# Optimization experiments

Measured on AMD Instinct MI355X. Metric: run time of the kernel, lower is better.

The kernel has to match this reference:

```python
import jax, jax.numpy as jnp
import numpy as np
import math

D_MODEL, N_HEAD, N_KV_HEAD, MAX_LEN = 2048, 32, 8, 2048
D_K = D_MODEL // N_HEAD
BASE = 10000.0
B, T = 2, 2048


def _rope_tables(seq_len):
    # matches torch Rotary: cos/sin of shape [seq_len, D_K], repeat_interleave(2) over freq dim
    inv_freq = 1.0 / (BASE ** (jnp.arange(0, D_K, 2, dtype=jnp.float32) / D_K))
    t = jnp.arange(seq_len, dtype=jnp.float32)[:, None] * inv_freq  # [T, D_K/2]
    cos = jnp.repeat(jnp.cos(t), 2, axis=-1)  # [T, D_K]
    sin = jnp.repeat(jnp.sin(t), 2, axis=-1)
    return cos, sin


def _rotate_half(x):
    # faithful to source: x1 = even lanes, x2 = odd lanes, concat([-x2, x1], -1)
    x1, x2 = x[..., ::2], x[..., 1::2]
    return jnp.concatenate([-x2, x1], axis=-1)


def _apply_rope(x, cos, sin):
    return x * cos + _rotate_half(x) * sin


def setup_inputs() -> dict:
    key = jax.random.key(0)
    ks = jax.random.split(key, 5)
    s = 1.0 / math.sqrt(D_MODEL)
    x = jax.random.normal(ks[0], (B, T, D_MODEL), dtype=jnp.float32)
    Wq = jax.random.normal(ks[1], (D_MODEL, N_HEAD * D_K), dtype=jnp.float32) * s
    Wk = jax.random.normal(ks[2], (D_MODEL, N_KV_HEAD * D_K), dtype=jnp.float32) * s
    Wv = jax.random.normal(ks[3], (D_MODEL, N_KV_HEAD * D_K), dtype=jnp.float32) * s
    Wo = jax.random.normal(ks[4], (N_HEAD * D_K, D_MODEL), dtype=jnp.float32) * s
    mask = jnp.tril(jnp.ones((T, T), dtype=bool))  # causal
    return {"x": x, "mask": mask, "Wq": Wq, "Wk": Wk, "Wv": Wv, "Wo": Wo}


def reference(x, mask, Wq, Wk, Wv, Wo):
    b, t, _ = x.shape
    g = N_HEAD // N_KV_HEAD
    q = (x @ Wq).reshape(b, t, N_HEAD, D_K).transpose(0, 2, 1, 3)      # [B,H,T,d]
    k = (x @ Wk).reshape(b, t, N_KV_HEAD, D_K).transpose(0, 2, 1, 3)   # [B,Hkv,T,d]
    v = (x @ Wv).reshape(b, t, N_KV_HEAD, D_K).transpose(0, 2, 1, 3)
    cos, sin = _rope_tables(t)
    q = _apply_rope(q, cos, sin)
    k = _apply_rope(k, cos, sin)  # rope before/after repeat is identical per-head
    # grouped attention: q head h attends kv head h // g (repeat_interleave semantics)
    qg = q.reshape(b, N_KV_HEAD, g, t, D_K)
    scores = jnp.einsum("bkgtd,bksd->bkgts", qg, k) / math.sqrt(D_K)
    neg = jnp.finfo(scores.dtype).min
    scores = jnp.where(mask[None, None, None, :, :], scores, neg)
    attn = jax.nn.softmax(scores, axis=-1)
    out = jnp.einsum("bkgts,bksd->bkgtd", attn, v)
    out = out.reshape(b, N_HEAD, t, D_K).transpose(0, 2, 1, 3).reshape(b, t, N_HEAD * D_K)
    return out @ Wo
```

## Files before the change

kernel.cpp:

```cpp
#include <hip/hip_runtime.h>
#include <cstdint>
#include <cstddef>

typedef unsigned short u16;
typedef __attribute__((ext_vector_type(8))) short bf16x8;
typedef __attribute__((ext_vector_type(8))) unsigned short u16x8;
typedef __attribute__((ext_vector_type(4))) unsigned short u16x4;
typedef __attribute__((ext_vector_type(4))) float f32x4;

__device__ __forceinline__ unsigned short f2bf(float f) {
    union { float f; uint32_t u; } c; c.f = f;
    uint32_t u = c.u + 0x7fffu + ((c.u >> 16) & 1u);
    return (unsigned short)(u >> 16);
}
__device__ __forceinline__ float bf2f(unsigned short h) {
    union { uint32_t u; float f; } c; c.u = ((uint32_t)h) << 16;
    return c.f;
}
__device__ __forceinline__ uint32_t pkbf(float a, float b) {
    union { float f; uint32_t u; } x, y; x.f = a; y.f = b;
    return ((x.u + 0x8000u) >> 16) | ((y.u + 0x8000u) & 0xFFFF0000u);
}

#define GLDS16(g, l)                                                               \
    __builtin_amdgcn_global_load_lds((const __attribute__((address_space(1))) void*)(g), \
                                     (__attribute__((address_space(3))) void*)(l), 16, 0, 0)

__global__ __launch_bounds__(256) void cvt_x(const float* __restrict__ src,
                                             u16* __restrict__ dst) {
    int i = blockIdx.x * 256 + threadIdx.x;
    const float4* s = (const float4*)src + (size_t)i * 2;
    float4 a = s[0], b = s[1];
    u16x8 o;
    o[0] = f2bf(a.x); o[1] = f2bf(a.y); o[2] = f2bf(a.z); o[3] = f2bf(a.w);
    o[4] = f2bf(b.x); o[5] = f2bf(b.y); o[6] = f2bf(b.z); o[7] = f2bf(b.w);
    *(u16x8*)(dst + (size_t)i * 8) = o;
}

__global__ __launch_bounds__(256) void tcvt(const float* __restrict__ src,
                                            u16* __restrict__ dst, int C) {
    __shared__ u16 tile[32][33];
    const int t = threadIdx.x;
    const int bx = blockIdx.x, by = blockIdx.y;
    const int tr = t >> 3, tc = (t & 7) << 2;
    float4 f = *(const float4*)&src[(size_t)(by * 32 + tr) * C + bx * 32 + tc];
    tile[tr][tc + 0] = f2bf(f.x); tile[tr][tc + 1] = f2bf(f.y);
    tile[tr][tc + 2] = f2bf(f.z); tile[tr][tc + 3] = f2bf(f.w);
    __syncthreads();
    u16x4 o;
    o[0] = tile[tc + 0][tr]; o[1] = tile[tc + 1][tr];
    o[2] = tile[tc + 2][tr]; o[3] = tile[tc + 3][tr];
    *(u16x4*)&dst[(size_t)(bx * 32 + tr) * 2048 + by * 32 + tc] = o;
}

__global__ __launch_bounds__(256) void tcvt3(const float* __restrict__ Wq,
                                             const float* __restrict__ Wk,
                                             const float* __restrict__ Wv,
                                             u16* __restrict__ dst) {
    __shared__ u16 tile[32][33];
    const int t = threadIdx.x;
    const int bxg = blockIdx.x, by = blockIdx.y;
    const float* src; int C, nb; u16* dbase;
    if (bxg < 64)      { src = Wq; C = 2048; nb = bxg;      dbase = dst; }
    else if (bxg < 80) { src = Wk; C = 512;  nb = bxg - 64; dbase = dst + (size_t)2048 * 2048; }
    else               { src = Wv; C = 512;  nb = bxg - 80; dbase = dst + (size_t)2560 * 2048; }
    const int tr = t >> 3, tc = (t & 7) << 2;
    float4 f = *(const float4*)&src[(size_t)(by * 32 + tr) * C + nb * 32 + tc];
    tile[tr][tc + 0] = f2bf(f.x); tile[tr][tc + 1] = f2bf(f.y);
    tile[tr][tc + 2] = f2bf(f.z); tile[tr][tc + 3] = f2bf(f.w);
    __syncthreads();
    u16x4 o;
    o[0] = tile[tc + 0][tr]; o[1] = tile[tc + 1][tr];
    o[2] = tile[tc + 2][tr]; o[3] = tile[tc + 3][tr];
    *(u16x4*)&dbase[(size_t)(nb * 32 + tr) * 2048 + by * 32 + tc] = o;
}

template <int MODE>
__global__ __launch_bounds__(256) void gemm2(const u16* __restrict__ A,
                                             const u16* __restrict__ Bt,
                                             u16* __restrict__ oq, u16* __restrict__ ok,
                                             u16* __restrict__ ov, float* __restrict__ of) {
    __shared__ u16 As[128 * 32];
    __shared__ u16 Bs[128 * 32];
    const int t = threadIdx.x, w = t >> 6, lane = t & 63;
    const int l15 = lane & 15, quad = lane >> 4;
    const int m0 = blockIdx.y << 7, n0 = blockIdx.x << 7;
    const int K = 2048;
    const int c0 = w * 2, c1 = c0 + 1;
    const int ar0 = c0 * 16 + (lane >> 2), ar1 = c1 * 16 + (lane >> 2);
    const int ac = (lane & 3) << 3;
    const u16* Ap0 = A + (size_t)(m0 + ar0) * K + ac;
    const u16* Ap1 = A + (size_t)(m0 + ar1) * K + ac;
    const u16* Bp0 = Bt + (size_t)(n0 + ar0) * K + ac;
    const u16* Bp1 = Bt + (size_t)(n0 + ar1) * K + ac;
    const int wm = (w >> 1) << 6, wn = (w & 1) << 6;

    f32x4 acc[4][4] = {};

    for (int k0 = 0; k0 < K; k0 += 32) {
        GLDS16(Ap0 + k0, &As[c0 * 512]);
        GLDS16(Ap1 + k0, &As[c1 * 512]);
        GLDS16(Bp0 + k0, &Bs[c0 * 512]);
        GLDS16(Bp1 + k0, &Bs[c1 * 512]);
        __syncthreads();
        bf16x8 a[4], bfr[4];
#pragma unroll
        for (int mt = 0; mt < 4; ++mt)
            a[mt] = *(bf16x8*)&As[(wm + mt * 16 + l15) * 32 + quad * 8];
#pragma unroll
        for (int nt = 0; nt < 4; ++nt)
            bfr[nt] = *(bf16x8*)&Bs[(wn + nt * 16 + l15) * 32 + quad * 8];
#pragma unroll
        for (int mt = 0; mt < 4; ++mt)
#pragma unroll
            for (int nt = 0; nt < 4; ++nt)
                acc[mt][nt] = __builtin_amdgcn_mfma_f32_16x16x32_bf16(a[mt], bfr[nt], acc[mt][nt], 0, 0, 0);
        __syncthreads();
    }

    if constexpr (MODE == 0) {
        const int colbase = n0 + wn;
        const bool isv = (colbase >= 2560);
        float iv[4];
        if (!isv) {
#pragma unroll
            for (int nt = 0; nt < 4; ++nt)
                iv[nt] = exp2f(-0.4152410118609253f * (float)(nt * 8 + (l15 >> 1)));
        }
        const int map1 = (quad << 4) | ((2 * l15 + 1) & 15);
        const int map2 = (quad << 4) | ((2 * l15) & 15);
        const bool lo = (l15 < 8);
#pragma unroll
        for (int mt = 0; mt < 4; ++mt)
#pragma unroll
            for (int r = 0; r < 4; ++r) {
                const int row = m0 + wm + mt * 16 + quad * 4 + r;
                float v0 = acc[mt][0][r], v1 = acc[mt][1][r];
                float v2 = acc[mt][2][r], v3 = acc[mt][3][r];
                float o0 = v0, o1 = v1, o2 = v2, o3 = v3;
                if (!isv) {
                    float g1a = __shfl(v0, map1), g1b = __shfl(v1, map1);
                    float g1c = __shfl(v2, map1), g1d = __shfl(v3, map1);
                    float g2a = __shfl(v0, map2), g2b = __shfl(v1, map2);
                    float g2c = __shfl(v2, map2), g2d = __shfl(v3, map2);
                    float p0 = lo ? g1a : g1b;
                    float p1 = lo ? g1c : g1d;
                    float p2 = lo ? g2a : g2b;
                    float p3 = lo ? g2c : g2d;
                    const float tt = (float)(row & 2047);
                    float sn, cs;
                    __sincosf(tt * iv[0], &sn, &cs); o0 = v0 * cs - p0 * sn;
                    __sincosf(tt * iv[1], &sn, &cs); o1 = v1 * cs - p1 * sn;
                    __sincosf(tt * iv[2], &sn, &cs); o2 = v2 * cs + p2 * sn;
                    __sincosf(tt * iv[3], &sn, &cs); o3 = v3 * cs + p3 * sn;
                }
                float o[4] = {o0, o1, o2, o3};
                if (colbase < 2048) {
#pragma unroll
                    for (int nt = 0; nt < 4; ++nt)
                        oq[(size_t)row * 2048 + colbase + nt * 16 + l15] = f2bf(o[nt]);
                } else if (colbase < 2560) {
#pragma unroll
                    for (int nt = 0; nt < 4; ++nt)
                        ok[(size_t)row * 512 + colbase - 2048 + nt * 16 + l15] = f2bf(o[nt]);
                } else {
#pragma unroll
                    for (int nt = 0; nt < 4; ++nt)
                        ov[(size_t)(colbase - 2560 + nt * 16 + l15) * 4096 + row] = f2bf(o[nt]);
                }
            }
    } else {
#pragma unroll
        for (int mt = 0; mt < 4; ++mt)
#pragma unroll
            for (int nt = 0; nt < 4; ++nt)
#pragma unroll
                for (int r = 0; r < 4; ++r) {
                    int row = m0 + wm + mt * 16 + quad * 4 + r;
                    int col = n0 + wn + nt * 16 + l15;
                    of[(size_t)row * 2048 + col] = acc[mt][nt][r];
                }
    }
}

__global__ __launch_bounds__(256, 3) void attn4(const u16* __restrict__ q,
                                                const u16* __restrict__ k,
                                                const u16* __restrict__ vT,
                                                u16* __restrict__ att) {
    __shared__ u16 Ks[64 * 72];
    __shared__ u16 Vt[64 * 72];
    __shared__ u16 Pw[4][16 * 72];

    const int t = threadIdx.x, w = t >> 6, lane = t & 63;
    const int l15 = lane & 15, quad = lane >> 4;
    const int bx = blockIdx.x, kvh = blockIdx.y, b = blockIdx.z;
    const int h = kvh * 4 + w;
    const size_t rowbase = (size_t)b * 2048;
    const int sr = t >> 2, sd = (t & 3) << 4;
    u16* Pq = &Pw[w][0];
    const float SC = 0.125f * 1.4426950408889634f;

    const u16* kbase = &k[(rowbase + sr) * 512 + kvh * 64 + sd];
    const u16* vbase = &vT[(size_t)(kvh * 64 + sr) * 4096 + rowbase + sd];

    for (int grp = 0; grp < 2; ++grp) {
        const int g = grp ? (63 - bx) : bx;
        const int qbase = g * 32;
        const int ntiles = (g >> 1) + 1;

        bf16x8 aq[2][2];
#pragma unroll
        for (int mt = 0; mt < 2; ++mt)
#pragma unroll
            for (int kc = 0; kc < 2; ++kc)
                aq[mt][kc] = *(const bf16x8*)&q[(rowbase + qbase + mt * 16 + l15) * 2048 +
                                               h * 64 + kc * 32 + quad * 8];

        f32x4 acc[2][4] = {};
        float m_i[2] = {-INFINITY, -INFINITY};
        float l_i[2] = {0.f, 0.f};

        u16x8 pk0 = *(const u16x8*)kbase;
        u16x8 pk1 = *(const u16x8*)(kbase + 8);
        u16x8 pv0 = *(const u16x8*)vbase;
        u16x8 pv1 = *(const u16x8*)(vbase + 8);

        for (int kb = 0; kb < ntiles; ++kb) {
            __syncthreads();
            *(u16x8*)&Ks[sr * 72 + sd]     = pk0;
            *(u16x8*)&Ks[sr * 72 + sd + 8] = pk1;
            *(u16x8*)&Vt[sr * 72 + sd]     = pv0;
            *(u16x8*)&Vt[sr * 72 + sd + 8] = pv1;
            if (kb + 1 < ntiles) {
                const u16* kp = kbase + (size_t)(kb + 1) * 64 * 512;
                pk0 = *(const u16x8*)kp;
                pk1 = *(const u16x8*)(kp + 8);
                const u16* vp = vbase + (size_t)(kb + 1) * 64;
                pv0 = *(const u16x8*)vp;
                pv1 = *(const u16x8*)(vp + 8);
            }
            __syncthreads();

            f32x4 st[2][4] = {};
#pragma unroll
            for (int kt = 0; kt < 4; ++kt) {
                bf16x8 ak0 = *(bf16x8*)&Ks[(kt * 16 + l15) * 72 + quad * 8];
                bf16x8 ak1 = *(bf16x8*)&Ks[(kt * 16 + l15) * 72 + 32 + quad * 8];
                st[0][kt] = __builtin_amdgcn_mfma_f32_16x16x32_bf16(ak0, aq[0][0], st[0][kt], 0, 0, 0);
                st[0][kt] = __builtin_amdgcn_mfma_f32_16x16x32_bf16(ak1, aq[0][1], st[0][kt], 0, 0, 0);
                st[1][kt] = __builtin_amdgcn_mfma_f32_16x16x32_bf16(ak0, aq[1][0], st[1][kt], 0, 0, 0);
                st[1][kt] = __builtin_amdgcn_mfma_f32_16x16x32_bf16(ak1, aq[1][1], st[1][kt], 0, 0, 0);
            }
            const bool diag = (kb == ntiles - 1);

#pragma unroll
            for (int mt = 0; mt < 2; ++mt) {
                float sv[16];
#pragma unroll
                for (int kt = 0; kt < 4; ++kt)
#pragma unroll
                    for (int r = 0; r < 4; ++r) sv[kt * 4 + r] = st[mt][kt][r] * SC;
                if (diag) {
                    const int qg = qbase + mt * 16 + l15;
#pragma unroll
                    for (int kt = 0; kt < 4; ++kt)
#pragma unroll
                        for (int r = 0; r < 4; ++r) {
                            int key = kb * 64 + kt * 16 + quad * 4 + r;
                            if (key > qg) sv[kt * 4 + r] = -INFINITY;
                        }
                }
                float mx = sv[0];
#pragma unroll
                for (int i = 1; i < 16; ++i) mx = fmaxf(mx, sv[i]);
                mx = fmaxf(mx, __shfl_xor(mx, 16));
                mx = fmaxf(mx, __shfl_xor(mx, 32));
                float mnew = fmaxf(m_i[mt], mx);
                float sum = 0.f;
#pragma unroll
                for (int i = 0; i < 16; ++i) {
                    sv[i] = __builtin_amdgcn_exp2f(sv[i] - mnew);
                    sum += sv[i];
                }
                sum += __shfl_xor(sum, 16);
                sum += __shfl_xor(sum, 32);
                float alpha = __builtin_amdgcn_exp2f(m_i[mt] - mnew);
                l_i[mt] = l_i[mt] * alpha + sum;
                m_i[mt] = mnew;

#pragma unroll
                for (int kt = 0; kt < 4; ++kt) {
                    uint2 uu;
                    uu.x = pkbf(sv[kt * 4 + 0], sv[kt * 4 + 1]);
                    uu.y = pkbf(sv[kt * 4 + 2], sv[kt * 4 + 3]);
                    *(uint2*)&Pq[l15 * 72 + kt * 16 + quad * 4] = uu;
                }
                bf16x8 bp0 = *(bf16x8*)&Pq[l15 * 72 + quad * 8];
                bf16x8 bp1 = *(bf16x8*)&Pq[l15 * 72 + 32 + quad * 8];

#pragma unroll
                for (int dt = 0; dt < 4; ++dt) {
                    bf16x8 av0 = *(bf16x8*)&Vt[(dt * 16 + l15) * 72 + quad * 8];
                    bf16x8 av1 = *(bf16x8*)&Vt[(dt * 16 + l15) * 72 + 32 + quad * 8];
#pragma unroll
                    for (int r = 0; r < 4; ++r) acc[mt][dt][r] *= alpha;
                    acc[mt][dt] = __builtin_amdgcn_mfma_f32_16x16x32_bf16(av0, bp0, acc[mt][dt], 0, 0, 0);
                    acc[mt][dt] = __builtin_amdgcn_mfma_f32_16x16x32_bf16(av1, bp1, acc[mt][dt], 0, 0, 0);
                }
            }
        }

#pragma unroll
        for (int mt = 0; mt < 2; ++mt) {
            float inv = 1.0f / l_i[mt];
            size_t row = rowbase + qbase + mt * 16 + l15;
#pragma unroll
            for (int dt = 0; dt < 4; ++dt) {
                uint2 uu;
                uu.x = pkbf(acc[mt][dt][0] * inv, acc[mt][dt][1] * inv);
                uu.y = pkbf(acc[mt][dt][2] * inv, acc[mt][dt][3] * inv);
                *(uint2*)&att[row * 2048 + h * 64 + dt * 16 + quad * 4] = uu;
            }
        }
    }
}

extern "C" void kernel_launch(void* const* d_in, const int* in_sizes, int n_in,
                              void* d_out, int out_size, void* d_ws, size_t ws_size,
                              hipStream_t stream) {
    const float* x  = (const float*)d_in[0];
    const float* Wq = (const float*)d_in[2];
    const float* Wk = (const float*)d_in[3];
    const float* Wv = (const float*)d_in[4];
    const float* Wo = (const float*)d_in[5];
    float* out = (float*)d_out;

    u16* xb = (u16*)d_out;

    u16* q     = (u16*)d_ws;
    u16* kk    = q + (size_t)4096 * 2048;
    u16* vt    = kk + (size_t)4096 * 512;
    u16* wqkvt = vt + (size_t)4096 * 512;
    u16* att   = wqkvt;
    u16* wot   = kk;

    cvt_x<<<4096, 256, 0, stream>>>(x, xb);
    tcvt3<<<dim3(96, 64), 256, 0, stream>>>(Wq, Wk, Wv, wqkvt);
    gemm2<0><<<dim3(24, 32), 256, 0, stream>>>(xb, wqkvt, q, kk, vt, nullptr);
    attn4<<<dim3(32, 8, 2), 256, 0, stream>>>(q, kk, vt, att);
    tcvt<<<dim3(64, 64), 256, 0, stream>>>(Wo, wot, 2048);
    gemm2<1><<<dim3(16, 32), 256, 0, stream>>>(att, wot, nullptr, nullptr, nullptr, out);
}
```

Before: 333.9 us.

## Restructure attention into paired 16-row query groups and widen GEMM k-step

The attention kernel now gives each block two 16-row query groups (a short one and a long one, mirrored for causal balance) sharing a single K/V tile stream. This doubles the grid and raises occupancy bounds to 4 blocks per CU. The softmax scale is folded into Q at the projection epilogue, removing a per-score multiply. The GEMM loads two 32-wide k-chunks per barrier pair, halving synchronisation at the cost of double the LDS.

```diff
diff --git a/kernel.cpp b/kernel.cpp
--- a/kernel.cpp
+++ b/kernel.cpp
@@ -76,12 +76,12 @@
 }
 
 template <int MODE>
-__global__ __launch_bounds__(256) void gemm2(const u16* __restrict__ A,
+__global__ __launch_bounds__(256) void gemm3(const u16* __restrict__ A,
                                              const u16* __restrict__ Bt,
                                              u16* __restrict__ oq, u16* __restrict__ ok,
                                              u16* __restrict__ ov, float* __restrict__ of) {
-    __shared__ u16 As[128 * 32];
-    __shared__ u16 Bs[128 * 32];
+    __shared__ u16 As[2 * 128 * 32];
+    __shared__ u16 Bs[2 * 128 * 32];
     const int t = threadIdx.x, w = t >> 6, lane = t & 63;
     const int l15 = lane & 15, quad = lane >> 4;
     const int m0 = blockIdx.y << 7, n0 = blockIdx.x << 7;
@@ -97,30 +97,38 @@
 
     f32x4 acc[4][4] = {};
 
-    for (int k0 = 0; k0 < K; k0 += 32) {
-        GLDS16(Ap0 + k0, &As[c0 * 512]);
-        GLDS16(Ap1 + k0, &As[c1 * 512]);
-        GLDS16(Bp0 + k0, &Bs[c0 * 512]);
-        GLDS16(Bp1 + k0, &Bs[c1 * 512]);
+    for (int k0 = 0; k0 < K; k0 += 64) {
+#pragma unroll
+        for (int kc = 0; kc < 2; ++kc) {
+            GLDS16(Ap0 + k0 + kc * 32, &As[kc * 4096 + c0 * 512]);
+            GLDS16(Ap1 + k0 + kc * 32, &As[kc * 4096 + c1 * 512]);
+            GLDS16(Bp0 + k0 + kc * 32, &Bs[kc * 4096 + c0 * 512]);
+            GLDS16(Bp1 + k0 + kc * 32, &Bs[kc * 4096 + c1 * 512]);
+        }
         __syncthreads();
-        bf16x8 a[4], bfr[4];
-#pragma unroll
-        for (int mt = 0; mt < 4; ++mt)
-            a[mt] = *(bf16x8*)&As[(wm + mt * 16 + l15) * 32 + quad * 8];
-#pragma unroll
-        for (int nt = 0; nt < 4; ++nt)
-            bfr[nt] = *(bf16x8*)&Bs[(wn + nt * 16 + l15) * 32 + quad * 8];
-#pragma unroll
-        for (int mt = 0; mt < 4; ++mt)
+#pragma unroll
+        for (int kc = 0; kc < 2; ++kc) {
+            bf16x8 a[4], bfr[4];
+#pragma unroll
+            for (int mt = 0; mt < 4; ++mt)
+                a[mt] = *(bf16x8*)&As[kc * 4096 + (wm + mt * 16 + l15) * 32 + quad * 8];
 #pragma unroll
             for (int nt = 0; nt < 4; ++nt)
-                acc[mt][nt] = __builtin_amdgcn_mfma_f32_16x16x32_bf16(a[mt], bfr[nt], acc[mt][nt], 0, 0, 0);
+                bfr[nt] = *(bf16x8*)&Bs[kc * 4096 + (wn + nt * 16 + l15) * 32 + quad * 8];
+#pragma unroll
+            for (int mt = 0; mt < 4; ++mt)
+#pragma unroll
+                for (int nt = 0; nt < 4; ++nt)
+                    acc[mt][nt] = __builtin_amdgcn_mfma_f32_16x16x32_bf16(a[mt], bfr[nt], acc[mt][nt], 0, 0, 0);
+        }
         __syncthreads();
     }
 
     if constexpr (MODE == 0) {
+        const float SC = 0.125f * 1.4426950408889634f;
         const int colbase = n0 + wn;
         const bool isv = (colbase >= 2560);
+        const bool isq = (colbase < 2048);
         float iv[4];
         if (!isv) {
 #pragma unroll
@@ -153,9 +161,10 @@
                     __sincosf(tt * iv[1], &sn, &cs); o1 = v1 * cs - p1 * sn;
                     __sincosf(tt * iv[2], &sn, &cs); o2 = v2 * cs + p2 * sn;
                     __sincosf(tt * iv[3], &sn, &cs); o3 = v3 * cs + p3 * sn;
+                    if (isq) { o0 *= SC; o1 *= SC; o2 *= SC; o3 *= SC; }
                 }
                 float o[4] = {o0, o1, o2, o3};
-                if (colbase < 2048) {
+                if (isq) {
 #pragma unroll
                     for (int nt = 0; nt < 4; ++nt)
                         oq[(size_t)row * 2048 + colbase + nt * 16 + l15] = f2bf(o[nt]);
@@ -183,7 +192,63 @@
     }
 }
 
-__global__ __launch_bounds__(256, 3) void attn4(const u16* __restrict__ q,
+__device__ __forceinline__ void soft_pv(const f32x4 st[4], float& m_i, float& l_i,
+                                        f32x4 acc[4], u16* __restrict__ Pq,
+                                        const u16* __restrict__ Vt,
+                                        int l15, int quad, int qg, int keybase, bool diag) {
+    float sv[16];
+#pragma unroll
+    for (int kt = 0; kt < 4; ++kt)
+#pragma unroll
+        for (int r = 0; r < 4; ++r) sv[kt * 4 + r] = st[kt][r];
+    if (diag) {
+#pragma unroll
+        for (int kt = 0; kt < 4; ++kt)
+#pragma unroll
+            for (int r = 0; r < 4; ++r) {
+                int key = keybase + kt * 16 + quad * 4 + r;
+                if (key > qg) sv[kt * 4 + r] = -INFINITY;
+            }
+    }
+    float mx = sv[0];
+#pragma unroll
+    for (int i = 1; i < 16; ++i) mx = fmaxf(mx, sv[i]);
+    mx = fmaxf(mx, __shfl_xor(mx, 16));
+    mx = fmaxf(mx, __shfl_xor(mx, 32));
+    float mnew = fmaxf(m_i, mx);
+    float sum = 0.f;
+#pragma unroll
+    for (int i = 0; i < 16; ++i) {
+        sv[i] = __builtin_amdgcn_exp2f(sv[i] - mnew);
+        sum += sv[i];
+    }
+    sum += __shfl_xor(sum, 16);
+    sum += __shfl_xor(sum, 32);
+    float alpha = __builtin_amdgcn_exp2f(m_i - mnew);
+    l_i = l_i * alpha + sum;
+    m_i = mnew;
+
+#pragma unroll
+    for (int kt = 0; kt < 4; ++kt) {
+        uint2 uu;
+        uu.x = pkbf(sv[kt * 4 + 0], sv[kt * 4 + 1]);
+        uu.y = pkbf(sv[kt * 4 + 2], sv[kt * 4 + 3]);
+        *(uint2*)&Pq[l15 * 72 + kt * 16 + quad * 4] = uu;
+    }
+    bf16x8 bp0 = *(bf16x8*)&Pq[l15 * 72 + quad * 8];
+    bf16x8 bp1 = *(bf16x8*)&Pq[l15 * 72 + 32 + quad * 8];
+#pragma unroll
+    for (int dt = 0; dt < 4; ++dt) {
+        bf16x8 av0 = *(const bf16x8*)&Vt[(dt * 16 + l15) * 72 + quad * 8];
+        bf16x8 av1 = *(const bf16x8*)&Vt[(dt * 16 + l15) * 72 + 32 + quad * 8];
+#pragma unroll
+        for (int r = 0; r < 4; ++r) acc[dt][r] *= alpha;
+        acc[dt] = __builtin_amdgcn_mfma_f32_16x16x32_bf16(av0, bp0, acc[dt], 0, 0, 0);
+        acc[dt] = __builtin_amdgcn_mfma_f32_16x16x32_bf16(av1, bp1, acc[dt], 0, 0, 0);
+    }
+}
+
+__global__ __launch_bounds__(256, 4) void attn5(const u16* __restrict__ q,
                                                 const u16* __restrict__ k,
                                                 const u16* __restrict__ vT,
                                                 u16* __restrict__ att) {
@@ -198,129 +263,81 @@
     const size_t rowbase = (size_t)b * 2048;
     const int sr = t >> 2, sd = (t & 3) << 4;
     u16* Pq = &Pw[w][0];
-    const float SC = 0.125f * 1.4426950408889634f;
+
+    const int gA = bx, gB = 127 - bx;
+    const int qbA = gA << 4, qbB = gB << 4;
+    const int ntA = (gA >> 2) + 1, ntB = (gB >> 2) + 1;
+
+    bf16x8 aqA[2], aqB[2];
+#pragma unroll
+    for (int kc = 0; kc < 2; ++kc) {
+        aqA[kc] = *(const bf16x8*)&q[(rowbase + qbA + l15) * 2048 + h * 64 + kc * 32 + quad * 8];
+        aqB[kc] = *(const bf16x8*)&q[(rowbase + qbB + l15) * 2048 + h * 64 + kc * 32 + quad * 8];
+    }
+
+    f32x4 accA[4] = {}, accB[4] = {};
+    float mA = -INFINITY, lA = 0.f, mB = -INFINITY, lB = 0.f;
 
     const u16* kbase = &k[(rowbase + sr) * 512 + kvh * 64 + sd];
     const u16* vbase = &vT[(size_t)(kvh * 64 + sr) * 4096 + rowbase + sd];
 
-    for (int grp = 0; grp < 2; ++grp) {
-        const int g = grp ? (63 - bx) : bx;
-        const int qbase = g * 32;
-        const int ntiles = (g >> 1) + 1;
-
-        bf16x8 aq[2][2];
-#pragma unroll
-        for (int mt = 0; mt < 2; ++mt)
-#pragma unroll
-            for (int kc = 0; kc < 2; ++kc)
-                aq[mt][kc] = *(const bf16x8*)&q[(rowbase + qbase + mt * 16 + l15) * 2048 +
-                                               h * 64 + kc * 32 + quad * 8];
-
-        f32x4 acc[2][4] = {};
-        float m_i[2] = {-INFINITY, -INFINITY};
-        float l_i[2] = {0.f, 0.f};
-
-        u16x8 pk0 = *(const u16x8*)kbase;
-        u16x8 pk1 = *(const u16x8*)(kbase + 8);
-        u16x8 pv0 = *(const u16x8*)vbase;
-        u16x8 pv1 = *(const u16x8*)(vbase + 8);
-
-        for (int kb = 0; kb < ntiles; ++kb) {
-            __syncthreads();
-            *(u16x8*)&Ks[sr * 72 + sd]     = pk0;
-            *(u16x8*)&Ks[sr * 72 + sd + 8] = pk1;
-            *(u16x8*)&Vt[sr * 72 + sd]     = pv0;
-            *(u16x8*)&Vt[sr * 72 + sd + 8] = pv1;
-            if (kb + 1 < ntiles) {
-                const u16* kp = kbase + (size_t)(kb + 1) * 64 * 512;
-                pk0 = *(const u16x8*)kp;
-                pk1 = *(const u16x8*)(kp + 8);
-                const u16* vp = vbase + (size_t)(kb + 1) * 64;
-                pv0 = *(const u16x8*)vp;
-                pv1 = *(const u16x8*)(vp + 8);
+    u16x8 pk0 = *(const u16x8*)kbase;
+    u16x8 pk1 = *(const u16x8*)(kbase + 8);
+    u16x8 pv0 = *(const u16x8*)vbase;
+    u16x8 pv1 = *(const u16x8*)(vbase + 8);
+
+    for (int kb = 0; kb < ntB; ++kb) {
+        __syncthreads();
+        *(u16x8*)&Ks[sr * 72 + sd]     = pk0;
+        *(u16x8*)&Ks[sr * 72 + sd + 8] = pk1;
+        *(u16x8*)&Vt[sr * 72 + sd]     = pv0;
+        *(u16x8*)&Vt[sr * 72 + sd + 8] = pv1;
+        if (kb + 1 < ntB) {
+            const u16* kp = kbase + (size_t)(kb + 1) * 64 * 512;
+            pk0 = *(const u16x8*)kp;
+            pk1 = *(const u16x8*)(kp + 8);
+            const u16* vp = vbase + (size_t)(kb + 1) * 64;
+            pv0 = *(const u16x8*)vp;
+            pv1 = *(const u16x8*)(vp + 8);
+        }
+        __syncthreads();
+
+        const bool doA = (kb < ntA);
+        f32x4 stA[4] = {}, stB[4] = {};
+#pragma unroll
+        for (int kt = 0; kt < 4; ++kt) {
+            bf16x8 ak0 = *(bf16x8*)&Ks[(kt * 16 + l15) * 72 + quad * 8];
+            bf16x8 ak1 = *(bf16x8*)&Ks[(kt * 16 + l15) * 72 + 32 + quad * 8];
+            stB[kt] = __builtin_amdgcn_mfma_f32_16x16x32_bf16(ak0, aqB[0], stB[kt], 0, 0, 0);
+            stB[kt] = __builtin_amdgcn_mfma_f32_16x16x32_bf16(ak1, aqB[1], stB[kt], 0, 0, 0);
+            if (doA) {
+                stA[kt] = __builtin_amdgcn_mfma_f32_16x16x32_bf16(ak0, aqA[0], stA[kt], 0, 0, 0);
+                stA[kt] = __builtin_amdgcn_mfma_f32_16x16x32_bf16(ak1, aqA[1], stA[kt], 0, 0, 0);
             }
-            __syncthreads();
-
-            f32x4 st[2][4] = {};
-#pragma unroll
-            for (int kt = 0; kt < 4; ++kt) {
-                bf16x8 ak0 = *(bf16x8*)&Ks[(kt * 16 + l15) * 72 + quad * 8];
-                bf16x8 ak1 = *(bf16x8*)&Ks[(kt * 16 + l15) * 72 + 32 + quad * 8];
-                st[0][kt] = __builtin_amdgcn_mfma_f32_16x16x32_bf16(ak0, aq[0][0], st[0][kt], 0, 0, 0);
-                st[0][kt] = __builtin_amdgcn_mfma_f32_16x16x32_bf16(ak1, aq[0][1], st[0][kt], 0, 0, 0);
-                st[1][kt] = __builtin_amdgcn_mfma_f32_16x16x32_bf16(ak0, aq[1][0], st[1][kt], 0, 0, 0);
-                st[1][kt] = __builtin_amdgcn_mfma_f32_16x16x32_bf16(ak1, aq[1][1], st[1][kt], 0, 0, 0);
-            }
-            const bool diag = (kb == ntiles - 1);
-
-#pragma unroll
-            for (int mt = 0; mt < 2; ++mt) {
-                float sv[16];
-#pragma unroll
-                for (int kt = 0; kt < 4; ++kt)
-#pragma unroll
-                    for (int r = 0; r < 4; ++r) sv[kt * 4 + r] = st[mt][kt][r] * SC;
-                if (diag) {
-                    const int qg = qbase + mt * 16 + l15;
-#pragma unroll
-                    for (int kt = 0; kt < 4; ++kt)
-#pragma unroll
-                        for (int r = 0; r < 4; ++r) {
-                            int key = kb * 64 + kt * 16 + quad * 4 + r;
-                            if (key > qg) sv[kt * 4 + r] = -INFINITY;
-                        }
-                }
-                float mx = sv[0];
-#pragma unroll
-                for (int i = 1; i < 16; ++i) mx = fmaxf(mx, sv[i]);
-                mx = fmaxf(mx, __shfl_xor(mx, 16));
-                mx = fmaxf(mx, __shfl_xor(mx, 32));
-                float mnew = fmaxf(m_i[mt], mx);
-                float sum = 0.f;
-#pragma unroll
-                for (int i = 0; i < 16; ++i) {
-                    sv[i] = __builtin_amdgcn_exp2f(sv[i] - mnew);
-                    sum += sv[i];
-                }
-                sum += __shfl_xor(sum, 16);
-                sum += __shfl_xor(sum, 32);
-                float alpha = __builtin_amdgcn_exp2f(m_i[mt] - mnew);
-                l_i[mt] = l_i[mt] * alpha + sum;
-                m_i[mt] = mnew;
-
-#pragma unroll
-                for (int kt = 0; kt < 4; ++kt) {
-                    uint2 uu;
-                    uu.x = pkbf(sv[kt * 4 + 0], sv[kt * 4 + 1]);
-                    uu.y = pkbf(sv[kt * 4 + 2], sv[kt * 4 + 3]);
-                    *(uint2*)&Pq[l15 * 72 + kt * 16 + quad * 4] = uu;
-                }
-                bf16x8 bp0 = *(bf16x8*)&Pq[l15 * 72 + quad * 8];
-                bf16x8 bp1 = *(bf16x8*)&Pq[l15 * 72 + 32 + quad * 8];
-
-#pragma unroll
-                for (int dt = 0; dt < 4; ++dt) {
-                    bf16x8 av0 = *(bf16x8*)&Vt[(dt * 16 + l15) * 72 + quad * 8];
-                    bf16x8 av1 = *(bf16x8*)&Vt[(dt * 16 + l15) * 72 + 32 + quad * 8];
-#pragma unroll
-                    for (int r = 0; r < 4; ++r) acc[mt][dt][r] *= alpha;
-                    acc[mt][dt] = __builtin_amdgcn_mfma_f32_16x16x32_bf16(av0, bp0, acc[mt][dt], 0, 0, 0);
-                    acc[mt][dt] = __builtin_amdgcn_mfma_f32_16x16x32_bf16(av1, bp1, acc[mt][dt], 0, 0, 0);
-                }
-            }
-        }
-
-#pragma unroll
-        for (int mt = 0; mt < 2; ++mt) {
-            float inv = 1.0f / l_i[mt];
-            size_t row = rowbase + qbase + mt * 16 + l15;
-#pragma unroll
-            for (int dt = 0; dt < 4; ++dt) {
-                uint2 uu;
-                uu.x = pkbf(acc[mt][dt][0] * inv, acc[mt][dt][1] * inv);
-                uu.y = pkbf(acc[mt][dt][2] * inv, acc[mt][dt][3] * inv);
-                *(uint2*)&att[row * 2048 + h * 64 + dt * 16 + quad * 4] = uu;
-            }
+        }
+        soft_pv(stB, mB, lB, accB, Pq, Vt, l15, quad, qbB + l15, kb * 64, kb == ntB - 1);
+        if (doA)
+            soft_pv(stA, mA, lA, accA, Pq, Vt, l15, quad, qbA + l15, kb * 64, kb == ntA - 1);
+    }
+
+    {
+        float inv = 1.0f / lA;
+        size_t row = rowbase + qbA + l15;
+#pragma unroll
+        for (int dt = 0; dt < 4; ++dt) {
+            uint2 uu;
+            uu.x = pkbf(accA[dt][0] * inv, accA[dt][1] * inv);
+            uu.y = pkbf(accA[dt][2] * inv, accA[dt][3] * inv);
+            *(uint2*)&att[row * 2048 + h * 64 + dt * 16 + quad * 4] = uu;
+        }
+        inv = 1.0f / lB;
+        row = rowbase + qbB + l15;
+#pragma unroll
+        for (int dt = 0; dt < 4; ++dt) {
+            uint2 uu;
+            uu.x = pkbf(accB[dt][0] * inv, accB[dt][1] * inv);
+            uu.y = pkbf(accB[dt][2] * inv, accB[dt][3] * inv);
+            *(uint2*)&att[row * 2048 + h * 64 + dt * 16 + quad * 4] = uu;
         }
     }
 }
@@ -346,8 +363,8 @@
 
     cvt_x<<<4096, 256, 0, stream>>>(x, xb);
     tcvt3<<<dim3(96, 64), 256, 0, stream>>>(Wq, Wk, Wv, wqkvt);
-    gemm2<0><<<dim3(24, 32), 256, 0, stream>>>(xb, wqkvt, q, kk, vt, nullptr);
-    attn4<<<dim3(32, 8, 2), 256, 0, stream>>>(q, kk, vt, att);
+    gemm3<0><<<dim3(24, 32), 256, 0, stream>>>(xb, wqkvt, q, kk, vt, nullptr);
+    attn5<<<dim3(64, 8, 2), 256, 0, stream>>>(q, kk, vt, att);
     tcvt<<<dim3(64, 64), 256, 0, stream>>>(Wo, wot, 2048);
-    gemm2<1><<<dim3(16, 32), 256, 0, stream>>>(att, wot, nullptr, nullptr, nullptr, out);
-}
+    gemm3<1><<<dim3(16, 32), 256, 0, stream>>>(att, wot, nullptr, nullptr, nullptr, out);
+}
```

After: 427.9 us. 28.2% more time.

## Split attention into one query tile per block, fold softmax scale into Q

Applied to the files above, without the earlier changes.

The attention kernel now launches one block per 32-row query tile (64x8x2 grid) instead of pairing tiles g and 63-g inside a single block. Heaviest tiles are issued first, and the occupancy hint rises from 3 to 4 blocks. The softmax scale is folded into Q in the QKV GEMM epilogue before bf16 rounding, removing a multiply per score. V fragments are loaded once per key tile instead of once per query half, and the max/sum reductions become tree-shaped. The cost is more blocks, each with a less balanced workload, and a slight change in rounding because the scale is applied before the bf16 conversion.

```diff
diff --git a/kernel.cpp b/kernel.cpp
--- a/kernel.cpp
+++ b/kernel.cpp
@@ -119,8 +119,10 @@
     }
 
     if constexpr (MODE == 0) {
+        const float SC = 0.125f * 1.4426950408889634f;
         const int colbase = n0 + wn;
         const bool isv = (colbase >= 2560);
+        const bool isq = (colbase < 2048);
         float iv[4];
         if (!isv) {
 #pragma unroll
@@ -153,9 +155,10 @@
                     __sincosf(tt * iv[1], &sn, &cs); o1 = v1 * cs - p1 * sn;
                     __sincosf(tt * iv[2], &sn, &cs); o2 = v2 * cs + p2 * sn;
                     __sincosf(tt * iv[3], &sn, &cs); o3 = v3 * cs + p3 * sn;
+                    if (isq) { o0 *= SC; o1 *= SC; o2 *= SC; o3 *= SC; }
                 }
                 float o[4] = {o0, o1, o2, o3};
-                if (colbase < 2048) {
+                if (isq) {
 #pragma unroll
                     for (int nt = 0; nt < 4; ++nt)
                         oq[(size_t)row * 2048 + colbase + nt * 16 + l15] = f2bf(o[nt]);
@@ -183,7 +186,66 @@
     }
 }
 
-__global__ __launch_bounds__(256, 3) void attn4(const u16* __restrict__ q,
+__device__ __forceinline__ void soft_pv(const f32x4 st[4], float& m_i, float& l_i,
+                                        f32x4 acc[4], u16* __restrict__ Pq,
+                                        const bf16x8 av[4][2],
+                                        int l15, int quad, int qg, int keybase, bool diag) {
+    float sv[16];
+#pragma unroll
+    for (int kt = 0; kt < 4; ++kt)
+#pragma unroll
+        for (int r = 0; r < 4; ++r) sv[kt * 4 + r] = st[kt][r];
+    if (diag) {
+#pragma unroll
+        for (int kt = 0; kt < 4; ++kt)
+#pragma unroll
+            for (int r = 0; r < 4; ++r) {
+                int key = keybase + kt * 16 + quad * 4 + r;
+                if (key > qg) sv[kt * 4 + r] = -INFINITY;
+            }
+    }
+    float tm[8];
+#pragma unroll
+    for (int i = 0; i < 8; ++i) tm[i] = fmaxf(sv[i], sv[i + 8]);
+#pragma unroll
+    for (int i = 0; i < 4; ++i) tm[i] = fmaxf(tm[i], tm[i + 4]);
+    float mx = fmaxf(fmaxf(tm[0], tm[1]), fmaxf(tm[2], tm[3]));
+    mx = fmaxf(mx, __shfl_xor(mx, 16));
+    mx = fmaxf(mx, __shfl_xor(mx, 32));
+    float mnew = fmaxf(m_i, mx);
+#pragma unroll
+    for (int i = 0; i < 16; ++i) sv[i] = __builtin_amdgcn_exp2f(sv[i] - mnew);
+    float ts[8];
+#pragma unroll
+    for (int i = 0; i < 8; ++i) ts[i] = sv[i] + sv[i + 8];
+#pragma unroll
+    for (int i = 0; i < 4; ++i) ts[i] = ts[i] + ts[i + 4];
+    float sum = (ts[0] + ts[1]) + (ts[2] + ts[3]);
+    sum += __shfl_xor(sum, 16);
+    sum += __shfl_xor(sum, 32);
+    float alpha = __builtin_amdgcn_exp2f(m_i - mnew);
+    l_i = l_i * alpha + sum;
+    m_i = mnew;
+
+#pragma unroll
+    for (int kt = 0; kt < 4; ++kt) {
+        uint2 uu;
+        uu.x = pkbf(sv[kt * 4 + 0], sv[kt * 4 + 1]);
+        uu.y = pkbf(sv[kt * 4 + 2], sv[kt * 4 + 3]);
+        *(uint2*)&Pq[l15 * 72 + kt * 16 + quad * 4] = uu;
+    }
+    bf16x8 bp0 = *(bf16x8*)&Pq[l15 * 72 + quad * 8];
+    bf16x8 bp1 = *(bf16x8*)&Pq[l15 * 72 + 32 + quad * 8];
+#pragma unroll
+    for (int dt = 0; dt < 4; ++dt) {
+#pragma unroll
+        for (int r = 0; r < 4; ++r) acc[dt][r] *= alpha;
+        acc[dt] = __builtin_amdgcn_mfma_f32_16x16x32_bf16(av[dt][0], bp0, acc[dt], 0, 0, 0);
+        acc[dt] = __builtin_amdgcn_mfma_f32_16x16x32_bf16(av[dt][1], bp1, acc[dt], 0, 0, 0);
+    }
+}
+
+__global__ __launch_bounds__(256, 4) void attn7(const u16* __restrict__ q,
                                                 const u16* __restrict__ k,
                                                 const u16* __restrict__ vT,
                                                 u16* __restrict__ att) {
@@ -193,134 +255,84 @@
 
     const int t = threadIdx.x, w = t >> 6, lane = t & 63;
     const int l15 = lane & 15, quad = lane >> 4;
-    const int bx = blockIdx.x, kvh = blockIdx.y, b = blockIdx.z;
+    const int g = 63 - (int)blockIdx.x;
+    const int kvh = blockIdx.y, b = blockIdx.z;
     const int h = kvh * 4 + w;
     const size_t rowbase = (size_t)b * 2048;
     const int sr = t >> 2, sd = (t & 3) << 4;
     u16* Pq = &Pw[w][0];
-    const float SC = 0.125f * 1.4426950408889634f;
+
+    const int qbase = g << 5;
+    const int ntiles = (g >> 1) + 1;
+
+    bf16x8 aq[2][2];
+#pragma unroll
+    for (int mt = 0; mt < 2; ++mt)
+#pragma unroll
+        for (int kc = 0; kc < 2; ++kc)
+            aq[mt][kc] = *(const bf16x8*)&q[(rowbase + qbase + mt * 16 + l15) * 2048 +
+                                           h * 64 + kc * 32 + quad * 8];
+
+    f32x4 acc[2][4] = {};
+    float m_i[2] = {-INFINITY, -INFINITY};
+    float l_i[2] = {0.f, 0.f};
 
     const u16* kbase = &k[(rowbase + sr) * 512 + kvh * 64 + sd];
     const u16* vbase = &vT[(size_t)(kvh * 64 + sr) * 4096 + rowbase + sd];
 
-    for (int grp = 0; grp < 2; ++grp) {
-        const int g = grp ? (63 - bx) : bx;
-        const int qbase = g * 32;
-        const int ntiles = (g >> 1) + 1;
-
-        bf16x8 aq[2][2];
-#pragma unroll
-        for (int mt = 0; mt < 2; ++mt)
+    u16x8 pk0 = *(const u16x8*)kbase;
+    u16x8 pk1 = *(const u16x8*)(kbase + 8);
+    u16x8 pv0 = *(const u16x8*)vbase;
+    u16x8 pv1 = *(const u16x8*)(vbase + 8);
+
+    for (int kb = 0; kb < ntiles; ++kb) {
+        __syncthreads();
+        *(u16x8*)&Ks[sr * 72 + sd]     = pk0;
+        *(u16x8*)&Ks[sr * 72 + sd + 8] = pk1;
+        *(u16x8*)&Vt[sr * 72 + sd]     = pv0;
+        *(u16x8*)&Vt[sr * 72 + sd + 8] = pv1;
+        if (kb + 1 < ntiles) {
+            const u16* kp = kbase + (size_t)(kb + 1) * 64 * 512;
+            pk0 = *(const u16x8*)kp;
+            pk1 = *(const u16x8*)(kp + 8);
+            const u16* vp = vbase + (size_t)(kb + 1) * 64;
+            pv0 = *(const u16x8*)vp;
+            pv1 = *(const u16x8*)(vp + 8);
+        }
+        __syncthreads();
+
+        bf16x8 av[4][2];
+#pragma unroll
+        for (int dt = 0; dt < 4; ++dt)
 #pragma unroll
             for (int kc = 0; kc < 2; ++kc)
-                aq[mt][kc] = *(const bf16x8*)&q[(rowbase + qbase + mt * 16 + l15) * 2048 +
-                                               h * 64 + kc * 32 + quad * 8];
-
-        f32x4 acc[2][4] = {};
-        float m_i[2] = {-INFINITY, -INFINITY};
-        float l_i[2] = {0.f, 0.f};
-
-        u16x8 pk0 = *(const u16x8*)kbase;
-        u16x8 pk1 = *(const u16x8*)(kbase + 8);
-        u16x8 pv0 = *(const u16x8*)vbase;
-        u16x8 pv1 = *(const u16x8*)(vbase + 8);
-
-        for (int kb = 0; kb < ntiles; ++kb) {
-            __syncthreads();
-            *(u16x8*)&Ks[sr * 72 + sd]     = pk0;
-            *(u16x8*)&Ks[sr * 72 + sd + 8] = pk1;
-            *(u16x8*)&Vt[sr * 72 + sd]     = pv0;
-            *(u16x8*)&Vt[sr * 72 + sd + 8] = pv1;
-            if (kb + 1 < ntiles) {
-                const u16* kp = kbase + (size_t)(kb + 1) * 64 * 512;
-                pk0 = *(const u16x8*)kp;
-                pk1 = *(const u16x8*)(kp + 8);
-                const u16* vp = vbase + (size_t)(kb + 1) * 64;
-                pv0 = *(const u16x8*)vp;
-                pv1 = *(const u16x8*)(vp + 8);
-            }
-            __syncthreads();
-
-            f32x4 st[2][4] = {};
-#pragma unroll
-            for (int kt = 0; kt < 4; ++kt) {
-                bf16x8 ak0 = *(bf16x8*)&Ks[(kt * 16 + l15) * 72 + quad * 8];
-                bf16x8 ak1 = *(bf16x8*)&Ks[(kt * 16 + l15) * 72 + 32 + quad * 8];
-                st[0][kt] = __builtin_amdgcn_mfma_f32_16x16x32_bf16(ak0, aq[0][0], st[0][kt], 0, 0, 0);
-                st[0][kt] = __builtin_amdgcn_mfma_f32_16x16x32_bf16(ak1, aq[0][1], st[0][kt], 0, 0, 0);
-                st[1][kt] = __builtin_amdgcn_mfma_f32_16x16x32_bf16(ak0, aq[1][0], st[1][kt], 0, 0, 0);
-                st[1][kt] = __builtin_amdgcn_mfma_f32_16x16x32_bf16(ak1, aq[1][1], st[1][kt], 0, 0, 0);
-            }
-            const bool diag = (kb == ntiles - 1);
-
-#pragma unroll
-            for (int mt = 0; mt < 2; ++mt) {
-                float sv[16];
-#pragma unroll
-                for (int kt = 0; kt < 4; ++kt)
-#pragma unroll
-                    for (int r = 0; r < 4; ++r) sv[kt * 4 + r] = st[mt][kt][r] * SC;
-                if (diag) {
-                    const int qg = qbase + mt * 16 + l15;
-#pragma unroll
-                    for (int kt = 0; kt < 4; ++kt)
-#pragma unroll
-                        for (int r = 0; r < 4; ++r) {
-                            int key = kb * 64 + kt * 16 + quad * 4 + r;
-                            if (key > qg) sv[kt * 4 + r] = -INFINITY;
-                        }
-                }
-                float mx = sv[0];
-#pragma unroll
-                for (int i = 1; i < 16; ++i) mx = fmaxf(mx, sv[i]);
-                mx = fmaxf(mx, __shfl_xor(mx, 16));
-                mx = fmaxf(mx, __shfl_xor(mx, 32));
-                float mnew = fmaxf(m_i[mt], mx);
-                float sum = 0.f;
-#pragma unroll
-                for (int i = 0; i < 16; ++i) {
-                    sv[i] = __builtin_amdgcn_exp2f(sv[i] - mnew);
-                    sum += sv[i];
-                }
-                sum += __shfl_xor(sum, 16);
-                sum += __shfl_xor(sum, 32);
-                float alpha = __builtin_amdgcn_exp2f(m_i[mt] - mnew);
-                l_i[mt] = l_i[mt] * alpha + sum;
-                m_i[mt] = mnew;
-
-#pragma unroll
-                for (int kt = 0; kt < 4; ++kt) {
-                    uint2 uu;
-                    uu.x = pkbf(sv[kt * 4 + 0], sv[kt * 4 + 1]);
-                    uu.y = pkbf(sv[kt * 4 + 2], sv[kt * 4 + 3]);
-                    *(uint2*)&Pq[l15 * 72 + kt * 16 + quad * 4] = uu;
-                }
-                bf16x8 bp0 = *(bf16x8*)&Pq[l15 * 72 + quad * 8];
-                bf16x8 bp1 = *(bf16x8*)&Pq[l15 * 72 + 32 + quad * 8];
-
-#pragma unroll
-                for (int dt = 0; dt < 4; ++dt) {
-                    bf16x8 av0 = *(bf16x8*)&Vt[(dt * 16 + l15) * 72 + quad * 8];
-                    bf16x8 av1 = *(bf16x8*)&Vt[(dt * 16 + l15) * 72 + 32 + quad * 8];
-#pragma unroll
-                    for (int r = 0; r < 4; ++r) acc[mt][dt][r] *= alpha;
-                    acc[mt][dt] = __builtin_amdgcn_mfma_f32_16x16x32_bf16(av0, bp0, acc[mt][dt], 0, 0, 0);
-                    acc[mt][dt] = __builtin_amdgcn_mfma_f32_16x16x32_bf16(av1, bp1, acc[mt][dt], 0, 0, 0);
-                }
-            }
+                av[dt][kc] = *(bf16x8*)&Vt[(dt * 16 + l15) * 72 + kc * 32 + quad * 8];
+
+        f32x4 st[2][4] = {};
+#pragma unroll
+        for (int kt = 0; kt < 4; ++kt) {
+            bf16x8 ak0 = *(bf16x8*)&Ks[(kt * 16 + l15) * 72 + quad * 8];
+            bf16x8 ak1 = *(bf16x8*)&Ks[(kt * 16 + l15) * 72 + 32 + quad * 8];
+            st[0][kt] = __builtin_amdgcn_mfma_f32_16x16x32_bf16(ak0, aq[0][0], st[0][kt], 0, 0, 0);
+            st[0][kt] = __builtin_amdgcn_mfma_f32_16x16x32_bf16(ak1, aq[0][1], st[0][kt], 0, 0, 0);
+            st[1][kt] = __builtin_amdgcn_mfma_f32_16x16x32_bf16(ak0, aq[1][0], st[1][kt], 0, 0, 0);
+            st[1][kt] = __builtin_amdgcn_mfma_f32_16x16x32_bf16(ak1, aq[1][1], st[1][kt], 0, 0, 0);
         }
-
-#pragma unroll
-        for (int mt = 0; mt < 2; ++mt) {
-            float inv = 1.0f / l_i[mt];
-            size_t row = rowbase + qbase + mt * 16 + l15;
-#pragma unroll
-            for (int dt = 0; dt < 4; ++dt) {
-                uint2 uu;
-                uu.x = pkbf(acc[mt][dt][0] * inv, acc[mt][dt][1] * inv);
-                uu.y = pkbf(acc[mt][dt][2] * inv, acc[mt][dt][3] * inv);
-                *(uint2*)&att[row * 2048 + h * 64 + dt * 16 + quad * 4] = uu;
-            }
+        const bool diag = (kb == ntiles - 1);
+        soft_pv(st[0], m_i[0], l_i[0], acc[0], Pq, av, l15, quad, qbase + l15, kb * 64, diag);
+        soft_pv(st[1], m_i[1], l_i[1], acc[1], Pq, av, l15, quad, qbase + 16 + l15, kb * 64, diag);
+    }
+
+#pragma unroll
+    for (int mt = 0; mt < 2; ++mt) {
+        float inv = 1.0f / l_i[mt];
+        size_t row = rowbase + qbase + mt * 16 + l15;
+#pragma unroll
+        for (int dt = 0; dt < 4; ++dt) {
+            uint2 uu;
+            uu.x = pkbf(acc[mt][dt][0] * inv, acc[mt][dt][1] * inv);
+            uu.y = pkbf(acc[mt][dt][2] * inv, acc[mt][dt][3] * inv);
+            *(uint2*)&att[row * 2048 + h * 64 + dt * 16 + quad * 4] = uu;
         }
     }
 }
@@ -347,7 +359,7 @@
     cvt_x<<<4096, 256, 0, stream>>>(x, xb);
     tcvt3<<<dim3(96, 64), 256, 0, stream>>>(Wq, Wk, Wv, wqkvt);
     gemm2<0><<<dim3(24, 32), 256, 0, stream>>>(xb, wqkvt, q, kk, vt, nullptr);
-    attn4<<<dim3(32, 8, 2), 256, 0, stream>>>(q, kk, vt, att);
+    attn7<<<dim3(64, 8, 2), 256, 0, stream>>>(q, kk, vt, att);
     tcvt<<<dim3(64, 64), 256, 0, stream>>>(Wo, wot, 2048);
     gemm2<1><<<dim3(16, 32), 256, 0, stream>>>(att, wot, nullptr, nullptr, nullptr, out);
 }
```

Result: slower. 587.4 us (+75.9%).
